# Kernel optimization log

Measured on AMD Instinct MI355X. Metric: run time of the kernel, lower is better.

## Reference

```python
import jax, jax.numpy as jnp
import numpy as np

N = 30000; E = 480000; B = 60
IN = 200; ID = 128; H = 128
NEXP = 4; TOPK = 2; TEMP = 1.5
HEADS = 4; DH = H // HEADS


def _ln(x, g, b):
    mu = jnp.mean(x, -1, keepdims=True)
    var = jnp.var(x, -1, keepdims=True)
    return (x - mu) / jnp.sqrt(var + 1e-5) * g + b


def _seg_sum(d, i, n):
    return jax.ops.segment_sum(d, i, num_segments=n)


def setup_inputs():
    key = jax.random.key(0)
    kit = iter(jax.random.split(key, 80))
    def w(*s):
        return jax.random.normal(next(kit), s, jnp.float32) * 0.05
    inp = {}
    inp['x'] = jax.random.normal(next(kit), (N, IN), jnp.float32)
    inp['node_identity'] = jax.random.normal(next(kit), (N, ID), jnp.float32)
    inp['edge_index'] = jax.random.randint(next(kit), (2, E), 0, N)
    inp['batch'] = jnp.sort(jax.random.randint(next(kit), (N,), 0, B))
    inp.update(fe_W=w(IN, H), fe_b=jnp.zeros(H), fe_g=jnp.ones(H), fe_be=jnp.zeros(H))
    inp.update(ie_W=w(ID, H), ie_b=jnp.zeros(H), ie_g=jnp.ones(H), ie_be=jnp.zeros(H))
    inp.update(fuse_W=w(2 * H, H), fuse_b=jnp.zeros(H), fuse_g=jnp.ones(H), fuse_be=jnp.zeros(H))
    inp.update(router_W=w(2 * H, NEXP))
    inp.update(mlp_W1=w(H, H), mlp_b1=jnp.zeros(H), mlp_W2=w(H, H), mlp_b2=jnp.zeros(H))
    inp.update(cheb_W=w(2, 2, H, H), cheb_b=jnp.zeros((2, H)))
    inp.update(gt_Wq=w(2, H, H), gt_bq=jnp.zeros((2, H)), gt_Wk=w(2, H, H), gt_bk=jnp.zeros((2, H)),
               gt_Wv=w(2, H, H), gt_bv=jnp.zeros((2, H)), gt_Ws=w(2, H, H), gt_bs=jnp.zeros((2, H)))
    inp.update(gcn_W=w(2, H, H), gcn_b=jnp.zeros((2, H)))
    inp.update(pn_g=jnp.ones((NEXP, H)), pn_b=jnp.zeros((NEXP, H)), expert_scales=jnp.ones(NEXP))
    inp.update(h1_W=w(H, H), h1_b=jnp.zeros(H), h1_g=jnp.ones(H), h1_be=jnp.zeros(H))
    inp.update(h2_W=w(H, H // 2), h2_b=jnp.zeros(H // 2), h2_g=jnp.ones(H // 2), h2_be=jnp.zeros(H // 2))
    inp.update(h3_W=w(H // 2, 2), h3_b=jnp.zeros(2), logit_bias=jnp.zeros(2))
    return inp


def _forward(x, node_identity, edge_index, batch, fe_W, fe_b, fe_g, fe_be, ie_W, ie_b, ie_g, ie_be,
             fuse_W, fuse_b, fuse_g, fuse_be, router_W, mlp_W1, mlp_b1, mlp_W2, mlp_b2, cheb_W, cheb_b,
             gt_Wq, gt_bq, gt_Wk, gt_bk, gt_Wv, gt_bv, gt_Ws, gt_bs, gcn_W, gcn_b, pn_g, pn_b,
             expert_scales, h1_W, h1_b, h1_g, h1_be, h2_W, h2_b, h2_g, h2_be, h3_W, h3_b, logit_bias):
    relu = jax.nn.relu
    src, dst = edge_index[0], edge_index[1]
    # encoders + fuse
    h_x = relu(_ln(x @ fe_W + fe_b, fe_g, fe_be))
    h_id = relu(_ln(node_identity @ ie_W + ie_b, ie_g, ie_be))
    h_router = jnp.concatenate([h_x, h_id], -1)
    h = relu(_ln(h_router @ fuse_W + fuse_b, fuse_g, fuse_be))
    # noisy top-k router (eval: no noise, no dropout)
    node_logits = h_router @ router_W
    probs = jax.nn.softmax(node_logits / TEMP, -1)
    vals, idx = jax.lax.top_k(probs, TOPK)
    wts = vals / jnp.clip(jnp.sum(vals, -1, keepdims=True), 1e-9)
    gates = jnp.zeros_like(probs).at[jnp.arange(N)[:, None], idx].set(wts)  # [N, 4]
    # degree / normalization terms
    ones_e = jnp.ones(E, jnp.float32)
    deg = _seg_sum(ones_e, dst, N)
    dinv = jnp.where(deg > 0, jax.lax.rsqrt(jnp.maximum(deg, 1.0)), 0.0)
    dinvl = jax.lax.rsqrt(deg + 1.0)  # with self loops (GCN)
    enorm = dinv[src] * dinv[dst]
    enorml = dinvl[src] * dinvl[dst]
    def aprop(xx, en, di_self=None):
        out = _seg_sum(xx[src] * en[:, None], dst, N)
        if di_self is not None:
            out = out + xx * di_self[:, None]
        return out
    # Expert 0: MLP (2 layers)
    e0 = relu(h @ mlp_W1 + mlp_b1) @ mlp_W2 + mlp_b2
    # Expert 1: ChebNet K=2 (lambda_max=2 -> L_hat = -A_norm), 2 layers
    z = h
    for l in range(2):
        tx1 = -aprop(z, enorm)
        z = z @ cheb_W[l, 0] + tx1 @ cheb_W[l, 1] + cheb_b[l]
        if l == 0:
            z = relu(z)
    e1 = z
    # Expert 2: Graph Transformer, 2 layers, heads=4, root-weight skip
    z = h
    for l in range(2):
        q = (z @ gt_Wq[l] + gt_bq[l]).reshape(N, HEADS, DH)
        k = (z @ gt_Wk[l] + gt_bk[l]).reshape(N, HEADS, DH)
        v = (z @ gt_Wv[l] + gt_bv[l]).reshape(N, HEADS, DH)
        logits = jnp.sum(q[dst] * k[src], -1) * (1.0 / DH ** 0.5)  # [E, heads]
        m = jax.ops.segment_max(logits, dst, num_segments=N)
        m = jnp.where(jnp.isfinite(m), m, 0.0)
        p = jnp.exp(logits - m[dst])
        denom = jnp.clip(_seg_sum(p, dst, N), 1e-9)
        attn = p / denom[dst]
        agg = _seg_sum(attn[:, :, None] * v[src], dst, N).reshape(N, H)
        z = agg + z @ gt_Ws[l] + gt_bs[l]
        if l == 0:
            z = relu(z)
    e2 = z
    # Expert 3: GCN, 2 layers, self loops
    z = h
    for l in range(2):
        zw = z @ gcn_W[l]
        z = aprop(zw, enorml, dinvl * dinvl) + gcn_b[l]
        if l == 0:
            z = relu(z)
    e3 = z
    # per-expert post-norm, scale, gated combine + residual
    eo = jnp.stack([e0, e1, e2, e3], 0)  # [4, N, H]
    eo = _ln(eo, pn_g[:, None, :], pn_b[:, None, :]) * expert_scales[:, None, None]
    out = h + jnp.einsum('ne,enh->nh', gates, eo)
    # mean-pool readout per graph
    counts = jnp.clip(_seg_sum(jnp.ones(N, jnp.float32), batch, B), 1.0)
    pooled = _seg_sum(out, batch, B) / counts[:, None]
    # classification head
    zc = relu(_ln(pooled @ h1_W + h1_b, h1_g, h1_be))
    zc = relu(_ln(zc @ h2_W + h2_b, h2_g, h2_be))
    return zc @ h3_W + h3_b + logit_bias


def reference(x, node_identity, edge_index, batch, fe_W, fe_b, fe_g, fe_be, ie_W, ie_b, ie_g, ie_be,
              fuse_W, fuse_b, fuse_g, fuse_be, router_W, mlp_W1, mlp_b1, mlp_W2, mlp_b2, cheb_W, cheb_b,
              gt_Wq, gt_bq, gt_Wk, gt_bk, gt_Wv, gt_bv, gt_Ws, gt_bs, gcn_W, gcn_b, pn_g, pn_b,
              expert_scales, h1_W, h1_b, h1_g, h1_be, h2_W, h2_b, h2_g, h2_be, h3_W, h3_b, logit_bias):
    return _forward(x, node_identity, edge_index, batch, fe_W, fe_b, fe_g, fe_be, ie_W, ie_b, ie_g, ie_be,
                    fuse_W, fuse_b, fuse_g, fuse_be, router_W, mlp_W1, mlp_b1, mlp_W2, mlp_b2, cheb_W, cheb_b,
                    gt_Wq, gt_bq, gt_Wk, gt_bk, gt_Wv, gt_bv, gt_Ws, gt_bs, gcn_W, gcn_b, pn_g, pn_b,
                    expert_scales, h1_W, h1_b, h1_g, h1_be, h2_W, h2_b, h2_g, h2_be, h3_W, h3_b, logit_bias)
```

## Files before the change

### kernel.cpp

```cpp
#include <hip/hip_runtime.h>

#define RELUF 1
#define ACCF  2
#define LNF   4
#define PCH   32
#define NWT   19
#define SCH   2048

typedef unsigned short ushort_t;
typedef __attribute__((ext_vector_type(8))) short bf16x8;
typedef __attribute__((ext_vector_type(4))) float f32x4;

__device__ __forceinline__ float bf2f(unsigned int v) {
    return __uint_as_float(v << 16);
}
__device__ __forceinline__ unsigned int f2bu(float f) {
    unsigned int u = __float_as_uint(f);
    return (u + 0x7fffu + ((u >> 16) & 1u)) >> 16;
}
__device__ __forceinline__ void unpack8(uint4 u, float* f) {
    f[0] = bf2f(u.x & 0xffff); f[1] = bf2f(u.x >> 16);
    f[2] = bf2f(u.y & 0xffff); f[3] = bf2f(u.y >> 16);
    f[4] = bf2f(u.z & 0xffff); f[5] = bf2f(u.z >> 16);
    f[6] = bf2f(u.w & 0xffff); f[7] = bf2f(u.w >> 16);
}
__device__ __forceinline__ uint4 pack8(const float* f) {
    uint4 p;
    p.x = f2bu(f[0]) | (f2bu(f[1]) << 16);
    p.y = f2bu(f[2]) | (f2bu(f[3]) << 16);
    p.z = f2bu(f[4]) | (f2bu(f[5]) << 16);
    p.w = f2bu(f[6]) | (f2bu(f[7]) << 16);
    return p;
}
__device__ __forceinline__ void fma8(uint4 u, float c, float* a) {
    a[0] = fmaf(c, bf2f(u.x & 0xffff), a[0]);
    a[1] = fmaf(c, bf2f(u.x >> 16), a[1]);
    a[2] = fmaf(c, bf2f(u.y & 0xffff), a[2]);
    a[3] = fmaf(c, bf2f(u.y >> 16), a[3]);
    a[4] = fmaf(c, bf2f(u.z & 0xffff), a[4]);
    a[5] = fmaf(c, bf2f(u.z >> 16), a[5]);
    a[6] = fmaf(c, bf2f(u.w & 0xffff), a[6]);
    a[7] = fmaf(c, bf2f(u.w >> 16), a[7]);
}
__device__ __forceinline__ float dot8(uint4 u, const float* q) {
    float d = q[0] * bf2f(u.x & 0xffff);
    d = fmaf(q[1], bf2f(u.x >> 16), d);
    d = fmaf(q[2], bf2f(u.y & 0xffff), d);
    d = fmaf(q[3], bf2f(u.y >> 16), d);
    d = fmaf(q[4], bf2f(u.z & 0xffff), d);
    d = fmaf(q[5], bf2f(u.z >> 16), d);
    d = fmaf(q[6], bf2f(u.w & 0xffff), d);
    d = fmaf(q[7], bf2f(u.w >> 16), d);
    return d;
}

__global__ void zero2_kernel(int* __restrict__ a, int na, int* __restrict__ b, int nb) {
    int i = blockIdx.x * blockDim.x + threadIdx.x;
    if (i < na) a[i] = 0;
    if (i < nb) b[i] = 0;
}
__global__ void seg_bounds_kernel(const int* __restrict__ batch, int* __restrict__ bstart,
                                  int* __restrict__ bend, int N) {
    int n = blockIdx.x * blockDim.x + threadIdx.x;
    if (n >= N) return;
    int b = batch[n];
    if (n == 0) bstart[b] = 0;
    else {
        int pb = batch[n - 1];
        if (pb != b) { bstart[b] = n; bend[pb] = n; }
    }
    if (n == N - 1) bend[b] = N;
}

__global__ void scan1_kernel(const int* __restrict__ degi, int* __restrict__ rowptr,
                             int* __restrict__ bsum, int n) {
    __shared__ int sh[256];
    int tid = threadIdx.x;
    int base = blockIdx.x * SCH + tid * 8;
    int loc[8]; int s = 0;
#pragma unroll
    for (int j = 0; j < 8; j++) {
        int idx = base + j;
        int v = (idx < n) ? degi[idx] : 0;
        s += v; loc[j] = s;
    }
    sh[tid] = s;
    __syncthreads();
    for (int off = 1; off < 256; off <<= 1) {
        int t = (tid >= off) ? sh[tid - off] : 0;
        __syncthreads();
        sh[tid] += t;
        __syncthreads();
    }
    int prev = (tid > 0) ? sh[tid - 1] : 0;
#pragma unroll
    for (int j = 0; j < 8; j++) {
        int idx = base + j;
        if (idx < n) rowptr[idx + 1] = prev + loc[j];
    }
    if (tid == 255) bsum[blockIdx.x] = sh[255];
}
__global__ void scan2_kernel(int* __restrict__ bsum, int nb) {
    __shared__ int sh[256];
    int tid = threadIdx.x;
    sh[tid] = (tid < nb) ? bsum[tid] : 0;
    __syncthreads();
    for (int off = 1; off < 256; off <<= 1) {
        int t = (tid >= off) ? sh[tid - off] : 0;
        __syncthreads();
        sh[tid] += t;
        __syncthreads();
    }
    if (tid < nb) bsum[tid] = (tid > 0) ? sh[tid - 1] : 0;
}
__global__ void scan3_kernel(int* __restrict__ rowptr, const int* __restrict__ bsum,
                             const int* __restrict__ degi,
                             float* __restrict__ dinv, float* __restrict__ dinvl, int n) {
    int i = blockIdx.x * blockDim.x + threadIdx.x;
    if (i == 0) rowptr[0] = 0;
    if (i < n) {
        rowptr[i + 1] += bsum[i / SCH];
        float deg = (float)degi[i];
        dinv[i] = (deg > 0.f) ? rsqrtf(fmaxf(deg, 1.f)) : 0.f;
        dinvl[i] = rsqrtf(deg + 1.f);
    }
}

struct WtPack {
    const float* src[NWT];
    unsigned long long off[NWT];
    int K[NWT];
};
__global__ void wconv_kernel(WtPack p, ushort_t* __restrict__ base) {
    int a = blockIdx.y;
    const float* s = p.src[a];
    ushort_t* d = base + p.off[a];
    int K = p.K[a];
    int total = K * 128;
    for (int i = blockIdx.x * blockDim.x + threadIdx.x; i < total; i += gridDim.x * blockDim.x) {
        int k = i >> 7, n = i & 127;
        d[n * K + k] = (ushort_t)f2bu(s[i]);
    }
}

__global__ __launch_bounds__(256)
void gemm_f32_ln_kernel(const float* __restrict__ A, int lda, int K,
                        const ushort_t* __restrict__ Wt,
                        ushort_t* __restrict__ Cb,
                        int M,
                        const float* __restrict__ bias,
                        const float* __restrict__ g, const float* __restrict__ be,
                        const float* __restrict__ rW,
                        float* __restrict__ logits)
{
    __shared__ ushort_t As[64][40];
    __shared__ ushort_t Bs[128][40];
    const int tid = threadIdx.x;
    const int m0 = blockIdx.x * 64;
    const int lane = tid & 63;
    const int wv = tid >> 6;
    const int q = lane >> 4;
    const int l16 = lane & 15;
    const int sar = tid >> 2;
    const int sak = (tid & 3) << 3;
    const int sbn = tid >> 1;
    const int sbk = (tid & 1) << 4;
    const bool arow_ok = (m0 + sar) < M;
    const float* Arow = A + (size_t)(m0 + sar) * lda;
    const ushort_t* Wrow = Wt + (size_t)sbn * K;

    f32x4 acc[8];
#pragma unroll
    for (int t = 0; t < 8; t++) acc[t] = (f32x4){0.f, 0.f, 0.f, 0.f};

    for (int k0 = 0; k0 < K; k0 += 32) {
        uint4 apk;
        if (arow_ok && k0 + sak + 8 <= K) {
            float4 p0 = *(const float4*)(Arow + k0 + sak);
            float4 p1 = *(const float4*)(Arow + k0 + sak + 4);
            apk.x = f2bu(p0.x) | (f2bu(p0.y) << 16);
            apk.y = f2bu(p0.z) | (f2bu(p0.w) << 16);
            apk.z = f2bu(p1.x) | (f2bu(p1.y) << 16);
            apk.w = f2bu(p1.z) | (f2bu(p1.w) << 16);
        } else {
            unsigned int t4[4] = {0, 0, 0, 0};
            for (int j = 0; j < 8; j++) {
                int k = k0 + sak + j;
                unsigned int bv = (arow_ok && k < K) ? f2bu(Arow[k]) : 0u;
                t4[j >> 1] |= bv << ((j & 1) * 16);
            }
            apk = make_uint4(t4[0], t4[1], t4[2], t4[3]);
        }
        uint4 b0, b1;
        if (k0 + sbk + 16 <= K) {
            b0 = *(const uint4*)(Wrow + k0 + sbk);
            b1 = *(const uint4*)(Wrow + k0 + sbk + 8);
        } else {
            unsigned int t8[8] = {0, 0, 0, 0, 0, 0, 0, 0};
            for (int j = 0; j < 16; j++) {
                int k = k0 + sbk + j;
                unsigned int bv = (k < K) ? (unsigned int)Wrow[k] : 0u;
                t8[j >> 1] |= bv << ((j & 1) * 16);
            }
            b0 = make_uint4(t8[0], t8[1], t8[2], t8[3]);
            b1 = make_uint4(t8[4], t8[5], t8[6], t8[7]);
        }
        __syncthreads();
        *(uint4*)&As[sar][sak] = apk;
        *(uint4*)&Bs[sbn][sbk] = b0;
        *(uint4*)&Bs[sbn][sbk + 8] = b1;
        __syncthreads();
        bf16x8 af = *(const bf16x8*)&As[16 * wv + l16][q * 8];
#pragma unroll
        for (int t = 0; t < 8; t++) {
            bf16x8 bf = *(const bf16x8*)&Bs[t * 16 + l16][q * 8];
            acc[t] = __builtin_amdgcn_mfma_f32_16x16x32_bf16(af, bf, acc[t], 0, 0, 0);
        }
    }
    const int row_base = m0 + 16 * wv + q * 4;
#pragma unroll
    for (int t = 0; t < 8; t++) {
        float bb = bias[t * 16 + l16];
#pragma unroll
        for (int r = 0; r < 4; r++) acc[t][r] += bb;
    }
    float mean[4], inv[4];
#pragma unroll
    for (int r = 0; r < 4; r++) {
        float s = 0.f, sq = 0.f;
#pragma unroll
        for (int t = 0; t < 8; t++) { float v = acc[t][r]; s += v; sq = fmaf(v, v, sq); }
#pragma unroll
        for (int off = 1; off <= 8; off <<= 1) { s += __shfl_xor(s, off); sq += __shfl_xor(sq, off); }
        mean[r] = s * (1.f / 128.f);
        float var = sq * (1.f / 128.f) - mean[r] * mean[r];
        inv[r] = rsqrtf(var + 1e-5f);
    }
    float rl0[4] = {0, 0, 0, 0}, rl1[4] = {0, 0, 0, 0};
    float rl2[4] = {0, 0, 0, 0}, rl3[4] = {0, 0, 0, 0};
#pragma unroll
    for (int t = 0; t < 8; t++) {
        int col = t * 16 + l16;
        float gg = g[col], b2 = be[col];
        float4 rw = *(const float4*)(rW + col * 4);
#pragma unroll
        for (int r = 0; r < 4; r++) {
            float y = fmaxf(fmaf((acc[t][r] - mean[r]) * inv[r], gg, b2), 0.f);
            rl0[r] = fmaf(y, rw.x, rl0[r]);
            rl1[r] = fmaf(y, rw.y, rl1[r]);
            rl2[r] = fmaf(y, rw.z, rl2[r]);
            rl3[r] = fmaf(y, rw.w, rl3[r]);
            float other = __shfl_xor(y, 1);
            int row = row_base + r;
            if (!(l16 & 1) && row < M) {
                unsigned int pk = f2bu(y) | (f2bu(other) << 16);
                *(unsigned int*)(Cb + (size_t)row * 256 + col) = pk;
            }
        }
    }
#pragma unroll
    for (int r = 0; r < 4; r++) {
#pragma unroll
        for (int off = 1; off <= 8; off <<= 1) {
            rl0[r] += __shfl_xor(rl0[r], off);
            rl1[r] += __shfl_xor(rl1[r], off);
            rl2[r] += __shfl_xor(rl2[r], off);
            rl3[r] += __shfl_xor(rl3[r], off);
        }
        int row = row_base + r;
        if (l16 == 0 && row < M)
            *(float4*)(logits + (size_t)row * 4) = make_float4(rl0[r], rl1[r], rl2[r], rl3[r]);
    }
}

template <int K>
__global__ __launch_bounds__(256)
void gemm_bf_kernel(const ushort_t* __restrict__ A,
                    const ushort_t* __restrict__ Wt,
                    ushort_t* __restrict__ Cb,
                    int M, const float* __restrict__ bias, int flags,
                    const float* __restrict__ g, const float* __restrict__ be)
{
    __shared__ ushort_t As[64][40];
    __shared__ ushort_t Bs[128][40];
    const int tid = threadIdx.x;
    const int m0 = blockIdx.x * 64;
    const int lane = tid & 63;
    const int wv = tid >> 6;
    const int q = lane >> 4;
    const int l16 = lane & 15;
    const int sar = tid >> 2;
    const int sak = (tid & 3) << 3;
    const int sbn = tid >> 1;
    const int sbk = (tid & 1) << 4;
    const bool arow_ok = (m0 + sar) < M;
    const ushort_t* Arow = A + (size_t)(m0 + sar) * K;
    const ushort_t* Wrow = Wt + (size_t)sbn * K;

    f32x4 acc[8];
#pragma unroll
    for (int t = 0; t < 8; t++) acc[t] = (f32x4){0.f, 0.f, 0.f, 0.f};

#pragma unroll
    for (int k0 = 0; k0 < K; k0 += 32) {
        uint4 apk = arow_ok ? *(const uint4*)(Arow + k0 + sak) : make_uint4(0, 0, 0, 0);
        uint4 b0 = *(const uint4*)(Wrow + k0 + sbk);
        uint4 b1 = *(const uint4*)(Wrow + k0 + sbk + 8);
        __syncthreads();
        *(uint4*)&As[sar][sak] = apk;
        *(uint4*)&Bs[sbn][sbk] = b0;
        *(uint4*)&Bs[sbn][sbk + 8] = b1;
        __syncthreads();
        bf16x8 af = *(const bf16x8*)&As[16 * wv + l16][q * 8];
#pragma unroll
        for (int t = 0; t < 8; t++) {
            bf16x8 bf = *(const bf16x8*)&Bs[t * 16 + l16][q * 8];
            acc[t] = __builtin_amdgcn_mfma_f32_16x16x32_bf16(af, bf, acc[t], 0, 0, 0);
        }
    }
    const int row_base = m0 + 16 * wv + q * 4;
    if (flags & LNF) {
#pragma unroll
        for (int t = 0; t < 8; t++) {
            float bb = bias[t * 16 + l16];
#pragma unroll
            for (int r = 0; r < 4; r++) acc[t][r] += bb;
        }
        float mean[4], inv[4];
#pragma unroll
        for (int r = 0; r < 4; r++) {
            float s = 0.f, sq = 0.f;
#pragma unroll
            for (int t = 0; t < 8; t++) { float v = acc[t][r]; s += v; sq = fmaf(v, v, sq); }
#pragma unroll
            for (int off = 1; off <= 8; off <<= 1) { s += __shfl_xor(s, off); sq += __shfl_xor(sq, off); }
            mean[r] = s * (1.f / 128.f);
            float var = sq * (1.f / 128.f) - mean[r] * mean[r];
            inv[r] = rsqrtf(var + 1e-5f);
        }
#pragma unroll
        for (int t = 0; t < 8; t++) {
            int col = t * 16 + l16;
            float gg = g[col], b2 = be[col];
#pragma unroll
            for (int r = 0; r < 4; r++) {
                float y = fmaf((acc[t][r] - mean[r]) * inv[r], gg, b2);
                if (flags & RELUF) y = fmaxf(y, 0.f);
                float other = __shfl_xor(y, 1);
                int row = row_base + r;
                if (!(l16 & 1) && row < M) {
                    unsigned int pk = f2bu(y) | (f2bu(other) << 16);
                    *(unsigned int*)(Cb + (size_t)row * 128 + col) = pk;
                }
            }
        }
        return;
    }
#pragma unroll
    for (int t = 0; t < 8; t++) {
        int col = t * 16 + l16;
        float bb = bias ? bias[col] : 0.f;
#pragma unroll
        for (int r = 0; r < 4; r++) {
            int row = row_base + r;
            bool ok = row < M;
            float val = acc[t][r] + bb;
            if ((flags & ACCF) && ok) val += bf2f(Cb[(size_t)row * 128 + col]);
            if (flags & RELUF) val = fmaxf(val, 0.f);
            float other = __shfl_xor(val, 1);
            if (!(lane & 1) && ok) {
                unsigned int pk = f2bu(val) | (f2bu(other) << 16);
                *(unsigned int*)(Cb + (size_t)row * 128 + col) = pk;
            }
        }
    }
}

__global__ __launch_bounds__(256)
void gemm_dual_kernel(const ushort_t* __restrict__ A1, const ushort_t* __restrict__ Wt1,
                      const ushort_t* __restrict__ A2, const ushort_t* __restrict__ Wt2,
                      ushort_t* __restrict__ Cb, int M,
                      const float* __restrict__ bias, int flags)
{
    const int K = 128;
    __shared__ ushort_t As[64][40];
    __shared__ ushort_t Bs[128][40];
    const int tid = threadIdx.x;
    const int m0 = blockIdx.x * 64;
    const int lane = tid & 63;
    const int wv = tid >> 6;
    const int q = lane >> 4;
    const int l16 = lane & 15;
    const int sar = tid >> 2;
    const int sak = (tid & 3) << 3;
    const int sbn = tid >> 1;
    const int sbk = (tid & 1) << 4;
    const bool arow_ok = (m0 + sar) < M;

    f32x4 acc[8];
#pragma unroll
    for (int t = 0; t < 8; t++) acc[t] = (f32x4){0.f, 0.f, 0.f, 0.f};

    for (int ph = 0; ph < 2; ph++) {
        const ushort_t* Arow = (ph ? A2 : A1) + (size_t)(m0 + sar) * K;
        const ushort_t* Wrow = (ph ? Wt2 : Wt1) + (size_t)sbn * K;
        for (int k0 = 0; k0 < K; k0 += 32) {
            uint4 apk = arow_ok ? *(const uint4*)(Arow + k0 + sak) : make_uint4(0, 0, 0, 0);
            uint4 b0 = *(const uint4*)(Wrow + k0 + sbk);
            uint4 b1 = *(const uint4*)(Wrow + k0 + sbk + 8);
            __syncthreads();
            *(uint4*)&As[sar][sak] = apk;
            *(uint4*)&Bs[sbn][sbk] = b0;
            *(uint4*)&Bs[sbn][sbk + 8] = b1;
            __syncthreads();
            bf16x8 af = *(const bf16x8*)&As[16 * wv + l16][q * 8];
#pragma unroll
            for (int t = 0; t < 8; t++) {
                bf16x8 bf = *(const bf16x8*)&Bs[t * 16 + l16][q * 8];
                acc[t] = __builtin_amdgcn_mfma_f32_16x16x32_bf16(af, bf, acc[t], 0, 0, 0);
            }
        }
    }
#pragma unroll
    for (int t = 0; t < 8; t++) {
        int col = t * 16 + l16;
        float bb = bias ? bias[col] : 0.f;
#pragma unroll
        for (int r = 0; r < 4; r++) {
            int row = m0 + 16 * wv + q * 4 + r;
            bool ok = row < M;
            float val = acc[t][r] + bb;
            if (flags & RELUF) val = fmaxf(val, 0.f);
            float other = __shfl_xor(val, 1);
            if (!(lane & 1) && ok) {
                unsigned int pk = f2bu(val) | (f2bu(other) << 16);
                *(unsigned int*)(Cb + (size_t)row * 128 + col) = pk;
            }
        }
    }
}

__global__ __launch_bounds__(256)
void gemm4_kernel(const ushort_t* __restrict__ A,
                  const ushort_t* __restrict__ Wt,
                  ushort_t* __restrict__ qb,
                  ushort_t* __restrict__ kv,
                  ushort_t* __restrict__ sk,
                  int M,
                  const float* __restrict__ b0, const float* __restrict__ b1,
                  const float* __restrict__ b2, const float* __restrict__ b3)
{
    const int K = 128;
    __shared__ ushort_t As[64][40];
    __shared__ ushort_t Bs[512][40];
    const int tid = threadIdx.x;
    const int m0 = blockIdx.x * 64;
    const int lane = tid & 63;
    const int wv = tid >> 6;
    const int q = lane >> 4;
    const int l16 = lane & 15;
    const int sar = tid >> 2;
    const int sak = (tid & 3) << 3;
    const bool arow_ok = (m0 + sar) < M;
    const ushort_t* Arow = A + (size_t)(m0 + sar) * K;

    f32x4 acc[32];
#pragma unroll
    for (int t = 0; t < 32; t++) acc[t] = (f32x4){0.f, 0.f, 0.f, 0.f};

    for (int k0 = 0; k0 < K; k0 += 32) {
        uint4 apk = arow_ok ? *(const uint4*)(Arow + k0 + sak) : make_uint4(0, 0, 0, 0);
        uint4 bv[4][2];
        int rows[4], kofs[4];
#pragma unroll
        for (int j = 0; j < 4; j++) {
            int slot = tid + j * 256;
            rows[j] = slot >> 1;
            kofs[j] = (slot & 1) << 4;
            const ushort_t* Wrow = Wt + (size_t)rows[j] * K + k0 + kofs[j];
            bv[j][0] = *(const uint4*)Wrow;
            bv[j][1] = *(const uint4*)(Wrow + 8);
        }
        __syncthreads();
        *(uint4*)&As[sar][sak] = apk;
#pragma unroll
        for (int j = 0; j < 4; j++) {
            *(uint4*)&Bs[rows[j]][kofs[j]] = bv[j][0];
            *(uint4*)&Bs[rows[j]][kofs[j] + 8] = bv[j][1];
        }
        __syncthreads();
        bf16x8 af = *(const bf16x8*)&As[16 * wv + l16][q * 8];
#pragma unroll
        for (int t = 0; t < 32; t++) {
            bf16x8 bf = *(const bf16x8*)&Bs[t * 16 + l16][q * 8];
            acc[t] = __builtin_amdgcn_mfma_f32_16x16x32_bf16(af, bf, acc[t], 0, 0, 0);
        }
    }
    const float* bs4[4] = {b0, b1, b2, b3};
#pragma unroll
    for (int s = 0; s < 4; s++) {
#pragma unroll
        for (int t8 = 0; t8 < 8; t8++) {
            int t = s * 8 + t8;
            int col = t8 * 16 + l16;
            float bb = bs4[s][col];
#pragma unroll
            for (int r = 0; r < 4; r++) {
                int row = m0 + 16 * wv + q * 4 + r;
                bool ok = row < M;
                float val = acc[t][r] + bb;
                float other = __shfl_xor(val, 1);
                if (!(lane & 1) && ok) {
                    unsigned int pk = f2bu(val) | (f2bu(other) << 16);
                    if (s == 0)
                        *(unsigned int*)(qb + (size_t)row * 128 + col) = pk;
                    else if (s == 3)
                        *(unsigned int*)(sk + (size_t)row * 128 + col) = pk;
                    else
                        *(unsigned int*)(kv + (size_t)row * 256 + (s - 1) * 128 + col) = pk;
                }
            }
        }
    }
}

__global__ void topk_kernel(const float* __restrict__ la, const float* __restrict__ lb,
                            float* __restrict__ gates, int M)
{
    int n = blockIdx.x * blockDim.x + threadIdx.x;
    if (n >= M) return;
    float4 a = *(const float4*)(la + (size_t)n * 4);
    float4 b = *(const float4*)(lb + (size_t)n * 4);
    float l[4] = {(a.x + b.x) * (1.f / 1.5f), (a.y + b.y) * (1.f / 1.5f),
                  (a.z + b.z) * (1.f / 1.5f), (a.w + b.w) * (1.f / 1.5f)};
    float mx = fmaxf(fmaxf(l[0], l[1]), fmaxf(l[2], l[3]));
    float e[4], ssum = 0.f;
#pragma unroll
    for (int i = 0; i < 4; i++) { e[i] = expf(l[i] - mx); ssum += e[i]; }
    float p[4];
#pragma unroll
    for (int i = 0; i < 4; i++) p[i] = e[i] / ssum;
    int i0 = 0;
    for (int i = 1; i < 4; i++) if (p[i] > p[i0]) i0 = i;
    int i1 = -1;
    for (int i = 0; i < 4; i++) {
        if (i == i0) continue;
        if (i1 < 0 || p[i] > p[i1]) i1 = i;
    }
    float wsum = fmaxf(p[i0] + p[i1], 1e-9f);
    float gg[4] = {0.f, 0.f, 0.f, 0.f};
    gg[i0] = p[i0] / wsum;
    gg[i1] = p[i1] / wsum;
    *(float4*)(gates + (size_t)n * 4) = make_float4(gg[0], gg[1], gg[2], gg[3]);
}

__global__ void edge_deg_kernel(const int* __restrict__ dst, int* __restrict__ degi, int E) {
    int e = blockIdx.x * blockDim.x + threadIdx.x;
    if (e < E) atomicAdd(&degi[dst[e]], 1);
}
__global__ void csr_fill_kernel(const int* __restrict__ src, const int* __restrict__ dst,
                                const int* __restrict__ rowptr, int* __restrict__ cursor,
                                int* __restrict__ csr,
                                const float* __restrict__ dinv, const float* __restrict__ dinvl,
                                float* __restrict__ ecA, float* __restrict__ ecB, int E) {
    int e = blockIdx.x * blockDim.x + threadIdx.x;
    if (e >= E) return;
    int d = dst[e];
    int s = src[e];
    int pos = atomicAdd(&cursor[d], 1);
    int o = rowptr[d] + pos;
    csr[o] = s;
    ecA[o] = dinv[d] * dinv[s];
    ecB[o] = dinvl[d] * dinvl[s];
}

__global__ void gather2_kernel(const ushort_t* __restrict__ Xb,
                               ushort_t* __restrict__ OutA, ushort_t* __restrict__ OutB,
                               const int* __restrict__ rowptr, const int* __restrict__ csr,
                               const float* __restrict__ ecA, const float* __restrict__ ecB,
                               const float* __restrict__ dinvl, int M)
{
    int node = blockIdx.x * 4 + (threadIdx.x >> 6);
    int lane = threadIdx.x & 63;
    if (node >= M) return;
    int beg = rowptr[node], end = rowptr[node + 1];
    int slot = lane >> 4, g = lane & 15;
    float aA[8] = {0, 0, 0, 0, 0, 0, 0, 0};
    float aB[8] = {0, 0, 0, 0, 0, 0, 0, 0};
    int s0 = 0, s1 = 0;
    float cA0 = 0.f, cB0 = 0.f, cA1 = 0.f, cB1 = 0.f;
    {
        int r0 = beg + slot, r1 = beg + 4 + slot;
        if (r0 < end) { s0 = csr[r0]; cA0 = ecA[r0]; cB0 = ecB[r0]; }
        if (r1 < end) { s1 = csr[r1]; cA1 = ecA[r1]; cB1 = ecB[r1]; }
    }
    for (int e = beg; e < end; e += 8) {
        int ns0 = 0, ns1 = 0;
        float nA0 = 0.f, nB0 = 0.f, nA1 = 0.f, nB1 = 0.f;
        int nr0 = e + 8 + slot, nr1 = e + 12 + slot;
        if (nr0 < end) { ns0 = csr[nr0]; nA0 = ecA[nr0]; nB0 = ecB[nr0]; }
        if (nr1 < end) { ns1 = csr[nr1]; nA1 = ecA[nr1]; nB1 = ecB[nr1]; }
        uint4 x0 = *(const uint4*)(Xb + (size_t)s0 * 128 + g * 8);
        uint4 x1 = *(const uint4*)(Xb + (size_t)s1 * 128 + g * 8);
        fma8(x0, cA0, aA); fma8(x0, cB0, aB);
        fma8(x1, cA1, aA); fma8(x1, cB1, aB);
        s0 = ns0; s1 = ns1;
        cA0 = nA0; cB0 = nB0; cA1 = nA1; cB1 = nB1;
    }
#pragma unroll
    for (int j = 0; j < 8; j++) {
        aA[j] += __shfl_xor(aA[j], 16); aA[j] += __shfl_xor(aA[j], 32);
        aB[j] += __shfl_xor(aB[j], 16); aB[j] += __shfl_xor(aB[j], 32);
    }
    {
        float c = dinvl[node]; c *= c;
        uint4 xs = *(const uint4*)(Xb + (size_t)node * 128 + g * 8);
        fma8(xs, c, aB);
    }
    if (lane < 16) {
        float oA[8], oB[8];
#pragma unroll
        for (int j = 0; j < 8; j++) { oA[j] = -aA[j]; oB[j] = aB[j]; }
        size_t ofs = (size_t)node * 128 + g * 8;
        *(uint4*)(OutA + ofs) = pack8(oA);
        *(uint4*)(OutB + ofs) = pack8(oB);
    }
}

__global__ void gather_l2_kernel(const ushort_t* __restrict__ XA, const ushort_t* __restrict__ XB,
                                 ushort_t* __restrict__ OutA, ushort_t* __restrict__ OutB,
                                 const int* __restrict__ rowptr, const int* __restrict__ csr,
                                 const float* __restrict__ ecA, const float* __restrict__ ecB,
                                 const float* __restrict__ dinvl, int M)
{
    int node = blockIdx.x * 4 + (threadIdx.x >> 6);
    int lane = threadIdx.x & 63;
    if (node >= M) return;
    int beg = rowptr[node], end = rowptr[node + 1];
    int slot = lane >> 4, g = lane & 15;
    float aA[8] = {0, 0, 0, 0, 0, 0, 0, 0};
    float aB[8] = {0, 0, 0, 0, 0, 0, 0, 0};
    int s0 = 0, s1 = 0;
    float cA0 = 0.f, cB0 = 0.f, cA1 = 0.f, cB1 = 0.f;
    {
        int r0 = beg + slot, r1 = beg + 4 + slot;
        if (r0 < end) { s0 = csr[r0]; cA0 = ecA[r0]; cB0 = ecB[r0]; }
        if (r1 < end) { s1 = csr[r1]; cA1 = ecA[r1]; cB1 = ecB[r1]; }
    }
    for (int e = beg; e < end; e += 8) {
        int ns0 = 0, ns1 = 0;
        float nA0 = 0.f, nB0 = 0.f, nA1 = 0.f, nB1 = 0.f;
        int nr0 = e + 8 + slot, nr1 = e + 12 + slot;
        if (nr0 < end) { ns0 = csr[nr0]; nA0 = ecA[nr0]; nB0 = ecB[nr0]; }
        if (nr1 < end) { ns1 = csr[nr1]; nA1 = ecA[nr1]; nB1 = ecB[nr1]; }
        uint4 a0 = *(const uint4*)(XA + (size_t)s0 * 128 + g * 8);
        uint4 a1 = *(const uint4*)(XA + (size_t)s1 * 128 + g * 8);
        uint4 b0 = *(const uint4*)(XB + (size_t)s0 * 128 + g * 8);
        uint4 b1 = *(const uint4*)(XB + (size_t)s1 * 128 + g * 8);
        fma8(a0, cA0, aA); fma8(a1, cA1, aA);
        fma8(b0, cB0, aB); fma8(b1, cB1, aB);
        s0 = ns0; s1 = ns1;
        cA0 = nA0; cB0 = nB0; cA1 = nA1; cB1 = nB1;
    }
#pragma unroll
    for (int j = 0; j < 8; j++) {
        aA[j] += __shfl_xor(aA[j], 16); aA[j] += __shfl_xor(aA[j], 32);
        aB[j] += __shfl_xor(aB[j], 16); aB[j] += __shfl_xor(aB[j], 32);
    }
    {
        float c = dinvl[node]; c *= c;
        uint4 xs = *(const uint4*)(XB + (size_t)node * 128 + g * 8);
        fma8(xs, c, aB);
    }
    if (lane < 16) {
        float oA[8], oB[8];
#pragma unroll
        for (int j = 0; j < 8; j++) { oA[j] = -aA[j]; oB[j] = aB[j]; }
        size_t ofs = (size_t)node * 128 + g * 8;
        *(uint4*)(OutA + ofs) = pack8(oA);
        *(uint4*)(OutB + ofs) = pack8(oB);
    }
}

__global__ void gt_attn_kernel(const ushort_t* __restrict__ Qb, const ushort_t* __restrict__ KV,
                               const int* __restrict__ rowptr, const int* __restrict__ csr,
                               const ushort_t* __restrict__ sk, int relu,
                               ushort_t* __restrict__ Outb, int M)
{
    const float SCL = 0.17677669529663689f * 1.4426950408889634f;
    int node = blockIdx.x * 4 + (threadIdx.x >> 6);
    int lane = threadIdx.x & 63;
    if (node >= M) return;
    int beg = rowptr[node], end = rowptr[node + 1];
    int slot = lane >> 4, g = lane & 15;
    uint4 qv = *(const uint4*)(Qb + (size_t)node * 128 + g * 8);
    float qf[8];
    unpack8(qv, qf);
#pragma unroll
    for (int j = 0; j < 8; j++) qf[j] *= SCL;
    float ax[8] = {0, 0, 0, 0, 0, 0, 0, 0};
    float den = 0.f;
    for (int e = beg; e < end; e += 8) {
        int r0 = e + slot, r1 = e + 4 + slot;
        bool v0 = r0 < end, v1 = r1 < end;
        int s0 = 0, s1 = 0;
        if (v0) s0 = csr[r0];
        if (v1) s1 = csr[r1];
        const ushort_t* p0 = KV + (size_t)s0 * 256 + g * 8;
        const ushort_t* p1 = KV + (size_t)s1 * 256 + g * 8;
        uint4 k0 = *(const uint4*)p0;
        uint4 k1 = *(const uint4*)p1;
        uint4 u0 = *(const uint4*)(p0 + 128);
        uint4 u1 = *(const uint4*)(p1 + 128);
        float d0 = dot8(k0, qf);
        float d1 = dot8(k1, qf);
        d0 += __shfl_xor(d0, 1); d0 += __shfl_xor(d0, 2);
        d1 += __shfl_xor(d1, 1); d1 += __shfl_xor(d1, 2);
        float w0 = v0 ? exp2f(fminf(d0, 80.f)) : 0.f;
        float w1 = v1 ? exp2f(fminf(d1, 80.f)) : 0.f;
        den += w0 + w1;
        fma8(u0, w0, ax);
        fma8(u1, w1, ax);
    }
#pragma unroll
    for (int j = 0; j < 8; j++) {
        ax[j] += __shfl_xor(ax[j], 16); ax[j] += __shfl_xor(ax[j], 32);
    }
    den += __shfl_xor(den, 16); den += __shfl_xor(den, 32);
    float dd = fmaxf(den, 1e-9f);
    if (lane < 16) {
        uint4 sv = *(const uint4*)(sk + (size_t)node * 128 + g * 8);
        float sf[8];
        unpack8(sv, sf);
        float o[8];
#pragma unroll
        for (int j = 0; j < 8; j++) {
            float v = ax[j] / dd + sf[j];
            o[j] = relu ? fmaxf(v, 0.f) : v;
        }
        *(uint4*)(Outb + (size_t)node * 128 + g * 8) = pack8(o);
    }
}

__global__ void pool_combine_kernel(const ushort_t* __restrict__ hb,
                                    const ushort_t* __restrict__ e0, const ushort_t* __restrict__ e1,
                                    const ushort_t* __restrict__ e2, const ushort_t* __restrict__ e3,
                                    const float* __restrict__ gates,
                                    const float* __restrict__ png, const float* __restrict__ pnb,
                                    const float* __restrict__ esc,
                                    const int* __restrict__ bstart, const int* __restrict__ bend,
                                    float* __restrict__ partial)
{
    int b = blockIdx.x, c = blockIdx.y;
    int lane = threadIdx.x;
    int s0 = bstart[b], e0i = bend[b];
    const ushort_t* eps[4] = {e0, e1, e2, e3};
    float ga[4], gb[4], ba[4], bb[4], es[4];
#pragma unroll
    for (int ee = 0; ee < 4; ee++) {
        ga[ee] = png[ee * 128 + lane * 2];
        gb[ee] = png[ee * 128 + lane * 2 + 1];
        ba[ee] = pnb[ee * 128 + lane * 2];
        bb[ee] = pnb[ee * 128 + lane * 2 + 1];
        es[ee] = esc[ee];
    }
    float sx = 0.f, sy = 0.f;
    for (int n = s0 + c; n < e0i; n += PCH) {
        size_t ofs = (size_t)n * 128 + lane * 2;
        float4 gg = *(const float4*)(gates + (size_t)n * 4);
        float gv[4] = {gg.x, gg.y, gg.z, gg.w};
        unsigned int hu = *(const unsigned int*)(hb + ofs);
        float ox = bf2f(hu & 0xffff), oy = bf2f(hu >> 16);
#pragma unroll
        for (int ee = 0; ee < 4; ee++) {
            unsigned int u = *(const unsigned int*)(eps[ee] + ofs);
            float vx = bf2f(u & 0xffff), vy = bf2f(u >> 16);
            float su = vx + vy, sq = vx * vx + vy * vy;
#pragma unroll
            for (int off = 32; off; off >>= 1) { su += __shfl_xor(su, off); sq += __shfl_xor(sq, off); }
            float mean = su * (1.f / 128.f);
            float var = sq * (1.f / 128.f) - mean * mean;
            float inv = rsqrtf(var + 1e-5f);
            float cc = es[ee] * gv[ee];
            ox = fmaf(cc, (vx - mean) * inv * ga[ee] + ba[ee], ox);
            oy = fmaf(cc, (vy - mean) * inv * gb[ee] + bb[ee], oy);
        }
        sx += ox; sy += oy;
    }
    *(float2*)(partial + ((size_t)b * PCH + c) * 128 + lane * 2) = make_float2(sx, sy);
}

__global__ void head_kernel(const float* __restrict__ partial,
                            const int* __restrict__ bstart, const int* __restrict__ bend,
                            const float* __restrict__ h1W, const float* __restrict__ h1b,
                            const float* __restrict__ h1g, const float* __restrict__ h1be,
                            const float* __restrict__ h2W, const float* __restrict__ h2b,
                            const float* __restrict__ h2g, const float* __restrict__ h2be,
                            const float* __restrict__ h3W, const float* __restrict__ h3b,
                            const float* __restrict__ lbias,
                            float* __restrict__ out, int B)
{
    __shared__ float p[128], z[128];
    int b = blockIdx.x, t = threadIdx.x;
    float sum = 0.f;
#pragma unroll
    for (int c = 0; c < PCH; c++) sum += partial[((size_t)b * PCH + c) * 128 + t];
    float cnt = fmaxf((float)(bend[b] - bstart[b]), 1.f);
    p[t] = sum / cnt;
    __syncthreads();
    float a = h1b[t];
    for (int k = 0; k < 128; k++) a = fmaf(p[k], h1W[k * 128 + t], a);
    z[t] = a;
    __syncthreads();
    float s = 0.f, sq = 0.f;
    for (int k = 0; k < 128; k++) { float x = z[k]; s += x; sq += x * x; }
    float mean = s * (1.f / 128.f), var = sq * (1.f / 128.f) - mean * mean;
    float y = fmaxf((a - mean) * rsqrtf(var + 1e-5f) * h1g[t] + h1be[t], 0.f);
    __syncthreads();
    z[t] = y;
    __syncthreads();
    float a2 = 0.f;
    if (t < 64) {
        a2 = h2b[t];
        for (int k = 0; k < 128; k++) a2 = fmaf(z[k], h2W[k * 64 + t], a2);
    }
    __syncthreads();
    if (t < 64) p[t] = a2;
    __syncthreads();
    if (t < 2) {
        float s2 = 0.f, sq2 = 0.f;
        for (int k = 0; k < 64; k++) { float x = p[k]; s2 += x; sq2 += x * x; }
        float mean2 = s2 * (1.f / 64.f), var2 = sq2 * (1.f / 64.f) - mean2 * mean2;
        float inv2 = rsqrtf(var2 + 1e-5f);
        float o = h3b[t] + lbias[t];
        for (int k = 0; k < 64; k++) {
            float zc = fmaxf((p[k] - mean2) * inv2 * h2g[k] + h2be[k], 0.f);
            o = fmaf(zc, h3W[k * 2 + t], o);
        }
        out[b * 2 + t] = o;
    }
}

extern "C" void kernel_launch(void* const* d_in, const int* in_sizes, int n_in,
                              void* d_out, int out_size, void* d_ws, size_t ws_size,
                              hipStream_t stream)
{
    (void)ws_size; (void)n_in;
    const int N = in_sizes[3];
    const int E = in_sizes[2] / 2;
    const int B = out_size / 2;

    const int* ei = (const int*)d_in[2];
    const int* src = ei;
    const int* dst = ei + E;
    const int* batch = (const int*)d_in[3];

    const float* W[47];
    for (int i = 0; i < 47; i++) W[i] = (const float*)d_in[i];

    size_t fN = (size_t)N;
    float* gates   = (float*)d_ws;
    float* dinv    = gates + 4 * fN;
    float* dinvl   = dinv + fN;
    float* partial = dinvl + fN;
    float* logitsA = partial + (size_t)128 * B * PCH;
    float* logitsB = logitsA + 4 * fN;
    ushort_t* hb  = (ushort_t*)(logitsB + 4 * fN);
    ushort_t* e0b = hb + 128 * fN;
    ushort_t* e1b = e0b + 128 * fN;
    ushort_t* e2b = e1b + 128 * fN;
    ushort_t* e3b = e2b + 128 * fN;
    ushort_t* x0  = e3b + 128 * fN;
    ushort_t* x1  = x0 + 128 * fN;
    ushort_t* x2  = x1 + 128 * fN;
    ushort_t* x3  = x2 + 128 * fN;
    ushort_t* qb  = x3 + 128 * fN;
    ushort_t* kvb = qb + 128 * fN;
    ushort_t* hrb = kvb + 256 * fN;
    ushort_t* wt  = hrb + 256 * fN;
    WtPack wp;
    const float* wsrc[NWT] = {
        W[4], W[8], W[12], W[17], W[19],
        W[21], W[21] + 16384, W[21] + 32768, W[21] + 49152,
        W[23], W[25], W[27], W[29],
        W[23] + 16384, W[25] + 16384, W[27] + 16384, W[29] + 16384,
        W[31], W[31] + 16384
    };
    const int wk[NWT] = {200, 128, 256, 128, 128,
                         128, 128, 128, 128,
                         128, 128, 128, 128,
                         128, 128, 128, 128,
                         128, 128};
    unsigned long long woff[NWT];
    unsigned long long acc_off = 0;
    for (int i = 0; i < NWT; i++) {
        wp.src[i] = wsrc[i];
        wp.K[i] = wk[i];
        wp.off[i] = acc_off;
        woff[i] = acc_off;
        acc_off += (unsigned long long)128 * wk[i];
    }
    int* degi   = (int*)(wt + acc_off + 8);
    int* cursor = degi + N;
    int* rowptr = cursor + N;
    int* csr    = rowptr + (N + 1);
    int* bstart = csr + E;
    int* bend   = bstart + B;
    int* bsum   = bend + B;
    float* ecA  = (float*)(bsum + 256);
    float* ecB  = ecA + E;

    dim3 blk(256);
    int gN4 = (N + 3) / 4;
    dim3 gG((N + 63) / 64);
    int nsb = (N + SCH - 1) / SCH;

    wconv_kernel<<<dim3(32, NWT), blk, 0, stream>>>(wp, wt);
    zero2_kernel<<<(2 * N + 255) / 256, blk, 0, stream>>>(degi, 2 * N, bstart, 2 * B);
    seg_bounds_kernel<<<(N + 255) / 256, blk, 0, stream>>>(batch, bstart, bend, N);
    edge_deg_kernel<<<(E + 255) / 256, blk, 0, stream>>>(dst, degi, E);
    scan1_kernel<<<dim3(nsb), blk, 0, stream>>>(degi, rowptr, bsum, N);
    scan2_kernel<<<1, blk, 0, stream>>>(bsum, nsb);
    scan3_kernel<<<(N + 255) / 256, blk, 0, stream>>>(rowptr, bsum, degi, dinv, dinvl, N);
    csr_fill_kernel<<<(E + 255) / 256, blk, 0, stream>>>(src, dst, rowptr, cursor, csr,
                                                         dinv, dinvl, ecA, ecB, E);

    gemm_f32_ln_kernel<<<gG, blk, 0, stream>>>(W[0], 200, 200, wt + woff[0], hrb, N,
                                               W[5], W[6], W[7], W[16], logitsA);
    gemm_f32_ln_kernel<<<gG, blk, 0, stream>>>(W[1], 128, 128, wt + woff[1], hrb + 128, N,
                                               W[9], W[10], W[11], W[16] + 512, logitsB);
    topk_kernel<<<(N + 255) / 256, blk, 0, stream>>>(logitsA, logitsB, gates, N);
    gemm_bf_kernel<256><<<gG, blk, 0, stream>>>(hrb, wt + woff[2], hb, N,
                                                W[13], RELUF | LNF, W[14], W[15]);

    gemm_bf_kernel<128><<<gG, blk, 0, stream>>>(hb, wt + woff[3], x0, N, W[18], RELUF, 0, 0);
    gemm_bf_kernel<128><<<gG, blk, 0, stream>>>(x0, wt + woff[4], e0b, N, W[20], 0, 0, 0);

    gather2_kernel<<<gN4, blk, 0, stream>>>(hb, x1, x2, rowptr, csr, ecA, ecB, dinvl, N);

    gemm_dual_kernel<<<gG, blk, 0, stream>>>(hb, wt + woff[5], x1, wt + woff[6],
                                             x0, N, W[22], RELUF);
    gemm_bf_kernel<128><<<gG, blk, 0, stream>>>(x2, wt + woff[17], x1, N, W[32], RELUF, 0, 0);

    gather_l2_kernel<<<gN4, blk, 0, stream>>>(x0, x1, x3, x2, rowptr, csr, ecA, ecB, dinvl, N);

    gemm_dual_kernel<<<gG, blk, 0, stream>>>(x0, wt + woff[7], x3, wt + woff[8],
                                             e1b, N, W[22] + 128, 0);
    gemm_bf_kernel<128><<<gG, blk, 0, stream>>>(x2, wt + woff[18], e3b, N, W[32] + 128, 0, 0, 0);

    gemm4_kernel<<<gG, blk, 0, stream>>>(hb, wt + woff[9], qb, kvb, x3, N,
                                         W[24], W[26], W[28], W[30]);
    gt_attn_kernel<<<gN4, blk, 0, stream>>>(qb, kvb, rowptr, csr, x3, 1, x1, N);
    gemm4_kernel<<<gG, blk, 0, stream>>>(x1, wt + woff[13], qb, kvb, x3, N,
                                         W[24] + 128, W[26] + 128, W[28] + 128, W[30] + 128);
    gt_attn_kernel<<<gN4, blk, 0, stream>>>(qb, kvb, rowptr, csr, x3, 0, e2b, N);

    pool_combine_kernel<<<dim3(B, PCH), dim3(64), 0, stream>>>(
        hb, e0b, e1b, e2b, e3b, gates, W[33], W[34], W[35], bstart, bend, partial);
    head_kernel<<<dim3(B), dim3(128), 0, stream>>>(partial, bstart, bend,
        W[36], W[37], W[38], W[39],
        W[40], W[41], W[42], W[43],
        W[44], W[45], W[46],
        (float*)d_out, B);
}
```

Measured before the change: 580.5 us.

## Merge independent stages into horizontally fused mega-kernels to cut launches

Many small independent kernels (weight conversion, segment bounds, degree count, scan3 plus both encoder GEMMs, CSR fill plus top-k gating, the various expert GEMMs and gathers) are merged into a few kernels that pick their role from the block index. The launch sequence is reordered so that independent branches (GT layer-1 attention with the Chebyshev/GCN layer-2 gather, and the MLP/Cheb/GCN/GT GEMMs) share one launch. Zeroing moves to hipMemsetAsync. This is meant to cut launch overhead and idle tails between dependent launches, at the cost of larger shared memory in the mega GEMM kernels (a 512-row Bs tile), extra intermediate buffers, and possibly lower occupancy for the lighter branches.

```diff
diff --git a/kernel.cpp b/kernel.cpp
--- a/kernel.cpp
+++ b/kernel.cpp
@@ -1,8 +1,5 @@
 #include <hip/hip_runtime.h>
 
-#define RELUF 1
-#define ACCF  2
-#define LNF   4
 #define PCH   32
 #define NWT   19
 #define SCH   2048
@@ -54,22 +51,43 @@
     return d;
 }
 
-__global__ void zero2_kernel(int* __restrict__ a, int na, int* __restrict__ b, int nb) {
-    int i = blockIdx.x * blockDim.x + threadIdx.x;
-    if (i < na) a[i] = 0;
-    if (i < nb) b[i] = 0;
-}
-__global__ void seg_bounds_kernel(const int* __restrict__ batch, int* __restrict__ bstart,
-                                  int* __restrict__ bend, int N) {
-    int n = blockIdx.x * blockDim.x + threadIdx.x;
-    if (n >= N) return;
-    int b = batch[n];
-    if (n == 0) bstart[b] = 0;
-    else {
-        int pb = batch[n - 1];
-        if (pb != b) { bstart[b] = n; bend[pb] = n; }
-    }
-    if (n == N - 1) bend[b] = N;
+struct WtPack {
+    const float* src[NWT];
+    unsigned long long off[NWT];
+    int K[NWT];
+};
+
+__global__ void setup_mega_kernel(WtPack p, ushort_t* __restrict__ base,
+                                  const int* __restrict__ batch,
+                                  int* __restrict__ bstart, int* __restrict__ bend, int N,
+                                  const int* __restrict__ dst, int* __restrict__ degi, int E)
+{
+    int bx = blockIdx.x, tid = threadIdx.x;
+    int nseg = (N + 255) >> 8;
+    if (bx < 608) {
+        int a = bx >> 5, xp = bx & 31;
+        const float* s = p.src[a];
+        ushort_t* d = base + p.off[a];
+        int K = p.K[a];
+        int total = K * 128;
+        for (int i = xp * 256 + tid; i < total; i += 32 * 256) {
+            int k = i >> 7, n = i & 127;
+            d[n * K + k] = (ushort_t)f2bu(s[i]);
+        }
+    } else if (bx < 608 + nseg) {
+        int n = (bx - 608) * 256 + tid;
+        if (n >= N) return;
+        int b = batch[n];
+        if (n == 0) bstart[b] = 0;
+        else {
+            int pb = batch[n - 1];
+            if (pb != b) { bstart[b] = n; bend[pb] = n; }
+        }
+        if (n == N - 1) bend[b] = N;
+    } else {
+        int e = (bx - 608 - nseg) * 256 + tid;
+        if (e < E) atomicAdd(&degi[dst[e]], 1);
+    }
 }
 
 __global__ void scan1_kernel(const int* __restrict__ degi, int* __restrict__ rowptr,
@@ -113,50 +131,19 @@
     }
     if (tid < nb) bsum[tid] = (tid > 0) ? sh[tid - 1] : 0;
 }
-__global__ void scan3_kernel(int* __restrict__ rowptr, const int* __restrict__ bsum,
-                             const int* __restrict__ degi,
-                             float* __restrict__ dinv, float* __restrict__ dinvl, int n) {
-    int i = blockIdx.x * blockDim.x + threadIdx.x;
-    if (i == 0) rowptr[0] = 0;
-    if (i < n) {
-        rowptr[i + 1] += bsum[i / SCH];
-        float deg = (float)degi[i];
-        dinv[i] = (deg > 0.f) ? rsqrtf(fmaxf(deg, 1.f)) : 0.f;
-        dinvl[i] = rsqrtf(deg + 1.f);
-    }
-}
-
-struct WtPack {
-    const float* src[NWT];
-    unsigned long long off[NWT];
-    int K[NWT];
+
+struct EncCfg {
+    const float* A; int lda; int K;
+    const ushort_t* Wt; ushort_t* Cb;
+    const float* bias; const float* g; const float* be;
+    const float* rW; float* logits;
 };
-__global__ void wconv_kernel(WtPack p, ushort_t* __restrict__ base) {
-    int a = blockIdx.y;
-    const float* s = p.src[a];
-    ushort_t* d = base + p.off[a];
-    int K = p.K[a];
-    int total = K * 128;
-    for (int i = blockIdx.x * blockDim.x + threadIdx.x; i < total; i += gridDim.x * blockDim.x) {
-        int k = i >> 7, n = i & 127;
-        d[n * K + k] = (ushort_t)f2bu(s[i]);
-    }
-}
-
-__global__ __launch_bounds__(256)
-void gemm_f32_ln_kernel(const float* __restrict__ A, int lda, int K,
-                        const ushort_t* __restrict__ Wt,
-                        ushort_t* __restrict__ Cb,
-                        int M,
-                        const float* __restrict__ bias,
-                        const float* __restrict__ g, const float* __restrict__ be,
-                        const float* __restrict__ rW,
-                        float* __restrict__ logits)
-{
-    __shared__ ushort_t As[64][40];
-    __shared__ ushort_t Bs[128][40];
+
+__device__ __forceinline__ void gemm_f32_ln_dev(ushort_t (*As)[40], ushort_t (*Bs)[40],
+                                                const EncCfg c, int bx, int M)
+{
     const int tid = threadIdx.x;
-    const int m0 = blockIdx.x * 64;
+    const int m0 = bx * 64;
     const int lane = tid & 63;
     const int wv = tid >> 6;
     const int q = lane >> 4;
@@ -165,9 +152,10 @@
     const int sak = (tid & 3) << 3;
     const int sbn = tid >> 1;
     const int sbk = (tid & 1) << 4;
+    const int K = c.K;
     const bool arow_ok = (m0 + sar) < M;
-    const float* Arow = A + (size_t)(m0 + sar) * lda;
-    const ushort_t* Wrow = Wt + (size_t)sbn * K;
+    const float* Arow = c.A + (size_t)(m0 + sar) * c.lda;
+    const ushort_t* Wrow = c.Wt + (size_t)sbn * K;
 
     f32x4 acc[8];
 #pragma unroll
@@ -220,7 +208,7 @@
     const int row_base = m0 + 16 * wv + q * 4;
 #pragma unroll
     for (int t = 0; t < 8; t++) {
-        float bb = bias[t * 16 + l16];
+        float bb = c.bias[t * 16 + l16];
 #pragma unroll
         for (int r = 0; r < 4; r++) acc[t][r] += bb;
     }
@@ -241,8 +229,8 @@
 #pragma unroll
     for (int t = 0; t < 8; t++) {
         int col = t * 16 + l16;
-        float gg = g[col], b2 = be[col];
-        float4 rw = *(const float4*)(rW + col * 4);
+        float gg = c.g[col], b2 = c.be[col];
+        float4 rw = *(const float4*)(c.rW + col * 4);
 #pragma unroll
         for (int r = 0; r < 4; r++) {
             float y = fmaxf(fmaf((acc[t][r] - mean[r]) * inv[r], gg, b2), 0.f);
@@ -254,7 +242,7 @@
             int row = row_base + r;
             if (!(l16 & 1) && row < M) {
                 unsigned int pk = f2bu(y) | (f2bu(other) << 16);
-                *(unsigned int*)(Cb + (size_t)row * 256 + col) = pk;
+                *(unsigned int*)(c.Cb + (size_t)row * 256 + col) = pk;
             }
         }
     }
@@ -269,18 +257,94 @@
         }
         int row = row_base + r;
         if (l16 == 0 && row < M)
-            *(float4*)(logits + (size_t)row * 4) = make_float4(rl0[r], rl1[r], rl2[r], rl3[r]);
-    }
-}
-
-template <int K>
+            *(float4*)(c.logits + (size_t)row * 4) = make_float4(rl0[r], rl1[r], rl2[r], rl3[r]);
+    }
+}
+
 __global__ __launch_bounds__(256)
-void gemm_bf_kernel(const ushort_t* __restrict__ A,
-                    const ushort_t* __restrict__ Wt,
-                    ushort_t* __restrict__ Cb,
-                    int M, const float* __restrict__ bias, int flags,
-                    const float* __restrict__ g, const float* __restrict__ be)
-{
+void scan3_enc_kernel(int* __restrict__ rowptr, const int* __restrict__ bsum,
+                      const int* __restrict__ degi,
+                      float* __restrict__ dinv, float* __restrict__ dinvl, int N,
+                      EncCfg c0, EncCfg c1)
+{
+    __shared__ ushort_t As[64][40];
+    __shared__ ushort_t Bs[128][40];
+    int bx = blockIdx.x;
+    int ns3 = (N + 255) >> 8;
+    int gG = (N + 63) >> 6;
+    if (bx < ns3) {
+        int i = bx * 256 + threadIdx.x;
+        if (i == 0) rowptr[0] = 0;
+        if (i < N) {
+            rowptr[i + 1] += bsum[i / SCH];
+            float deg = (float)degi[i];
+            dinv[i] = (deg > 0.f) ? rsqrtf(fmaxf(deg, 1.f)) : 0.f;
+            dinvl[i] = rsqrtf(deg + 1.f);
+        }
+        return;
+    }
+    int b2 = bx - ns3;
+    if (b2 < gG) gemm_f32_ln_dev(As, Bs, c0, b2, N);
+    else gemm_f32_ln_dev(As, Bs, c1, b2 - gG, N);
+}
+
+__global__ void csr_topk_kernel(const int* __restrict__ src, const int* __restrict__ dst,
+                                const int* __restrict__ rowptr, int* __restrict__ cursor,
+                                int* __restrict__ csr,
+                                const float* __restrict__ dinv, const float* __restrict__ dinvl,
+                                float* __restrict__ ecA, float* __restrict__ ecB, int E,
+                                const float* __restrict__ la, const float* __restrict__ lb,
+                                float* __restrict__ gates, int N)
+{
+    int bx = blockIdx.x;
+    int nc = (E + 255) >> 8;
+    if (bx < nc) {
+        int e = bx * 256 + threadIdx.x;
+        if (e >= E) return;
+        int d = dst[e];
+        int s = src[e];
+        int pos = atomicAdd(&cursor[d], 1);
+        int o = rowptr[d] + pos;
+        csr[o] = s;
+        ecA[o] = dinv[d] * dinv[s];
+        ecB[o] = dinvl[d] * dinvl[s];
+        return;
+    }
+    int n = (bx - nc) * 256 + threadIdx.x;
+    if (n >= N) return;
+    float4 a = *(const float4*)(la + (size_t)n * 4);
+    float4 b = *(const float4*)(lb + (size_t)n * 4);
+    float l[4] = {(a.x + b.x) * (1.f / 1.5f), (a.y + b.y) * (1.f / 1.5f),
+                  (a.z + b.z) * (1.f / 1.5f), (a.w + b.w) * (1.f / 1.5f)};
+    float mx = fmaxf(fmaxf(l[0], l[1]), fmaxf(l[2], l[3]));
+    float e4[4], ssum = 0.f;
+#pragma unroll
+    for (int i = 0; i < 4; i++) { e4[i] = expf(l[i] - mx); ssum += e4[i]; }
+    float p[4];
+#pragma unroll
+    for (int i = 0; i < 4; i++) p[i] = e4[i] / ssum;
+    int i0 = 0;
+    for (int i = 1; i < 4; i++) if (p[i] > p[i0]) i0 = i;
+    int i1 = -1;
+    for (int i = 0; i < 4; i++) {
+        if (i == i0) continue;
+        if (i1 < 0 || p[i] > p[i1]) i1 = i;
+    }
+    float wsum = fmaxf(p[i0] + p[i1], 1e-9f);
+    float gg[4] = {0.f, 0.f, 0.f, 0.f};
+    gg[i0] = p[i0] / wsum;
+    gg[i1] = p[i1] / wsum;
+    *(float4*)(gates + (size_t)n * 4) = make_float4(gg[0], gg[1], gg[2], gg[3]);
+}
+
+__global__ __launch_bounds__(256)
+void gemm_ln256_kernel(const ushort_t* __restrict__ A,
+                       const ushort_t* __restrict__ Wt,
+                       ushort_t* __restrict__ Cb, int M,
+                       const float* __restrict__ bias,
+                       const float* __restrict__ g, const float* __restrict__ be)
+{
+    const int K = 256;
     __shared__ ushort_t As[64][40];
     __shared__ ushort_t Bs[128][40];
     const int tid = threadIdx.x;
@@ -319,42 +383,82 @@
         }
     }
     const int row_base = m0 + 16 * wv + q * 4;
-    if (flags & LNF) {
+#pragma unroll
+    for (int t = 0; t < 8; t++) {
+        float bb = bias[t * 16 + l16];
+#pragma unroll
+        for (int r = 0; r < 4; r++) acc[t][r] += bb;
+    }
+    float mean[4], inv[4];
+#pragma unroll
+    for (int r = 0; r < 4; r++) {
+        float s = 0.f, sq = 0.f;
+#pragma unroll
+        for (int t = 0; t < 8; t++) { float v = acc[t][r]; s += v; sq = fmaf(v, v, sq); }
+#pragma unroll
+        for (int off = 1; off <= 8; off <<= 1) { s += __shfl_xor(s, off); sq += __shfl_xor(sq, off); }
+        mean[r] = s * (1.f / 128.f);
+        float var = sq * (1.f / 128.f) - mean[r] * mean[r];
+        inv[r] = rsqrtf(var + 1e-5f);
+    }
+#pragma unroll
+    for (int t = 0; t < 8; t++) {
+        int col = t * 16 + l16;
+        float gg = g[col], b2 = be[col];
+#pragma unroll
+        for (int r = 0; r < 4; r++) {
+            float y = fmaxf(fmaf((acc[t][r] - mean[r]) * inv[r], gg, b2), 0.f);
+            float other = __shfl_xor(y, 1);
+            int row = row_base + r;
+            if (!(l16 & 1) && row < M) {
+                unsigned int pk = f2bu(y) | (f2bu(other) << 16);
+                *(unsigned int*)(Cb + (size_t)row * 128 + col) = pk;
+            }
+        }
+    }
+}
+
+template <int K>
+__device__ __forceinline__ void gemm_bf_dev(ushort_t (*As)[40], ushort_t (*Bs)[40],
+                                            const ushort_t* __restrict__ A,
+                                            const ushort_t* __restrict__ Wt,
+                                            ushort_t* __restrict__ Cb, int M,
+                                            const float* __restrict__ bias, int relu, int bx)
+{
+    const int tid = threadIdx.x;
+    const int m0 = bx * 64;
+    const int lane = tid & 63;
+    const int wv = tid >> 6;
+    const int q = lane >> 4;
+    const int l16 = lane & 15;
+    const int sar = tid >> 2;
+    const int sak = (tid & 3) << 3;
+    const int sbn = tid >> 1;
+    const int sbk = (tid & 1) << 4;
+    const bool arow_ok = (m0 + sar) < M;
+    const ushort_t* Arow = A + (size_t)(m0 + sar) * K;
+    const ushort_t* Wrow = Wt + (size_t)sbn * K;
+
+    f32x4 acc[8];
+#pragma unroll
+    for (int t = 0; t < 8; t++) acc[t] = (f32x4){0.f, 0.f, 0.f, 0.f};
+
+#pragma unroll
+    for (int k0 = 0; k0 < K; k0 += 32) {
+        uint4 apk = arow_ok ? *(const uint4*)(Arow + k0 + sak) : make_uint4(0, 0, 0, 0);
+        uint4 b0 = *(const uint4*)(Wrow + k0 + sbk);
+        uint4 b1 = *(const uint4*)(Wrow + k0 + sbk + 8);
+        __syncthreads();
+        *(uint4*)&As[sar][sak] = apk;
+        *(uint4*)&Bs[sbn][sbk] = b0;
+        *(uint4*)&Bs[sbn][sbk + 8] = b1;
+        __syncthreads();
+        bf16x8 af = *(const bf16x8*)&As[16 * wv + l16][q * 8];
 #pragma unroll
         for (int t = 0; t < 8; t++) {
-            float bb = bias[t * 16 + l16];
-#pragma unroll
-            for (int r = 0; r < 4; r++) acc[t][r] += bb;
-        }
-        float mean[4], inv[4];
-#pragma unroll
-        for (int r = 0; r < 4; r++) {
-            float s = 0.f, sq = 0.f;
-#pragma unroll
-            for (int t = 0; t < 8; t++) { float v = acc[t][r]; s += v; sq = fmaf(v, v, sq); }
-#pragma unroll
-            for (int off = 1; off <= 8; off <<= 1) { s += __shfl_xor(s, off); sq += __shfl_xor(sq, off); }
-            mean[r] = s * (1.f / 128.f);
-            float var = sq * (1.f / 128.f) - mean[r] * mean[r];
-            inv[r] = rsqrtf(var + 1e-5f);
-        }
-#pragma unroll
-        for (int t = 0; t < 8; t++) {
-            int col = t * 16 + l16;
-            float gg = g[col], b2 = be[col];
-#pragma unroll
-            for (int r = 0; r < 4; r++) {
-                float y = fmaf((acc[t][r] - mean[r]) * inv[r], gg, b2);
-                if (flags & RELUF) y = fmaxf(y, 0.f);
-                float other = __shfl_xor(y, 1);
-                int row = row_base + r;
-                if (!(l16 & 1) && row < M) {
-                    unsigned int pk = f2bu(y) | (f2bu(other) << 16);
-                    *(unsigned int*)(Cb + (size_t)row * 128 + col) = pk;
-                }
-            }
-        }
-        return;
+            bf16x8 bf = *(const bf16x8*)&Bs[t * 16 + l16][q * 8];
+            acc[t] = __builtin_amdgcn_mfma_f32_16x16x32_bf16(af, bf, acc[t], 0, 0, 0);
+        }
     }
 #pragma unroll
     for (int t = 0; t < 8; t++) {
@@ -362,13 +466,11 @@
         float bb = bias ? bias[col] : 0.f;
 #pragma unroll
         for (int r = 0; r < 4; r++) {
-            int row = row_base + r;
-            bool ok = row < M;
+            int row = m0 + 16 * wv + q * 4 + r;
             float val = acc[t][r] + bb;
-            if ((flags & ACCF) && ok) val += bf2f(Cb[(size_t)row * 128 + col]);
-            if (flags & RELUF) val = fmaxf(val, 0.f);
+            if (relu) val = fmaxf(val, 0.f);
             float other = __shfl_xor(val, 1);
-            if (!(lane & 1) && ok) {
+            if (!(lane & 1) && row < M) {
                 unsigned int pk = f2bu(val) | (f2bu(other) << 16);
                 *(unsigned int*)(Cb + (size_t)row * 128 + col) = pk;
             }
@@ -376,17 +478,17 @@
     }
 }
 
-__global__ __launch_bounds__(256)
-void gemm_dual_kernel(const ushort_t* __restrict__ A1, const ushort_t* __restrict__ Wt1,
-                      const ushort_t* __restrict__ A2, const ushort_t* __restrict__ Wt2,
-                      ushort_t* __restrict__ Cb, int M,
-                      const float* __restrict__ bias, int flags)
+__device__ __forceinline__ void gemm_dual_dev(ushort_t (*As)[40], ushort_t (*Bs)[40],
+                                              const ushort_t* __restrict__ A1,
+                                              const ushort_t* __restrict__ Wt1,
+                                              const ushort_t* __restrict__ A2,
+                                              const ushort_t* __restrict__ Wt2,
+                                              ushort_t* __restrict__ Cb, int M,
+                                              const float* __restrict__ bias, int relu, int bx)
 {
     const int K = 128;
-    __shared__ ushort_t As[64][40];
-    __shared__ ushort_t Bs[128][40];
     const int tid = threadIdx.x;
-    const int m0 = blockIdx.x * 64;
+    const int m0 = bx * 64;
     const int lane = tid & 63;
     const int wv = tid >> 6;
     const int q = lane >> 4;
@@ -428,11 +530,10 @@
 #pragma unroll
         for (int r = 0; r < 4; r++) {
             int row = m0 + 16 * wv + q * 4 + r;
-            bool ok = row < M;
             float val = acc[t][r] + bb;
-            if (flags & RELUF) val = fmaxf(val, 0.f);
+            if (relu) val = fmaxf(val, 0.f);
             float other = __shfl_xor(val, 1);
-            if (!(lane & 1) && ok) {
+            if (!(lane & 1) && row < M) {
                 unsigned int pk = f2bu(val) | (f2bu(other) << 16);
                 *(unsigned int*)(Cb + (size_t)row * 128 + col) = pk;
             }
@@ -440,21 +541,18 @@
     }
 }
 
-__global__ __launch_bounds__(256)
-void gemm4_kernel(const ushort_t* __restrict__ A,
-                  const ushort_t* __restrict__ Wt,
-                  ushort_t* __restrict__ qb,
-                  ushort_t* __restrict__ kv,
-                  ushort_t* __restrict__ sk,
-                  int M,
-                  const float* __restrict__ b0, const float* __restrict__ b1,
-                  const float* __restrict__ b2, const float* __restrict__ b3)
+__device__ __forceinline__ void gemm4_dev(ushort_t (*As)[40], ushort_t (*Bs)[40],
+                                          const ushort_t* __restrict__ A,
+                                          const ushort_t* __restrict__ Wt,
+                                          ushort_t* __restrict__ qb, ushort_t* __restrict__ kv,
+                                          ushort_t* __restrict__ sk, int M,
+                                          const float* __restrict__ b0, const float* __restrict__ b1,
+                                          const float* __restrict__ b2, const float* __restrict__ b3,
+                                          int bx)
 {
     const int K = 128;
-    __shared__ ushort_t As[64][40];
-    __shared__ ushort_t Bs[512][40];
     const int tid = threadIdx.x;
-    const int m0 = blockIdx.x * 64;
+    const int m0 = bx * 64;
     const int lane = tid & 63;
     const int wv = tid >> 6;
     const int q = lane >> 4;
@@ -507,10 +605,9 @@
 #pragma unroll
             for (int r = 0; r < 4; r++) {
                 int row = m0 + 16 * wv + q * 4 + r;
-                bool ok = row < M;
                 float val = acc[t][r] + bb;
                 float other = __shfl_xor(val, 1);
-                if (!(lane & 1) && ok) {
+                if (!(lane & 1) && row < M) {
                     unsigned int pk = f2bu(val) | (f2bu(other) << 16);
                     if (s == 0)
                         *(unsigned int*)(qb + (size_t)row * 128 + col) = pk;
@@ -524,63 +621,59 @@
     }
 }
 
-__global__ void topk_kernel(const float* __restrict__ la, const float* __restrict__ lb,
-                            float* __restrict__ gates, int M)
-{
-    int n = blockIdx.x * blockDim.x + threadIdx.x;
-    if (n >= M) return;
-    float4 a = *(const float4*)(la + (size_t)n * 4);
-    float4 b = *(const float4*)(lb + (size_t)n * 4);
-    float l[4] = {(a.x + b.x) * (1.f / 1.5f), (a.y + b.y) * (1.f / 1.5f),
-                  (a.z + b.z) * (1.f / 1.5f), (a.w + b.w) * (1.f / 1.5f)};
-    float mx = fmaxf(fmaxf(l[0], l[1]), fmaxf(l[2], l[3]));
-    float e[4], ssum = 0.f;
-#pragma unroll
-    for (int i = 0; i < 4; i++) { e[i] = expf(l[i] - mx); ssum += e[i]; }
-    float p[4];
-#pragma unroll
-    for (int i = 0; i < 4; i++) p[i] = e[i] / ssum;
-    int i0 = 0;
-    for (int i = 1; i < 4; i++) if (p[i] > p[i0]) i0 = i;
-    int i1 = -1;
-    for (int i = 0; i < 4; i++) {
-        if (i == i0) continue;
-        if (i1 < 0 || p[i] > p[i1]) i1 = i;
-    }
-    float wsum = fmaxf(p[i0] + p[i1], 1e-9f);
-    float gg[4] = {0.f, 0.f, 0.f, 0.f};
-    gg[i0] = p[i0] / wsum;
-    gg[i1] = p[i1] / wsum;
-    *(float4*)(gates + (size_t)n * 4) = make_float4(gg[0], gg[1], gg[2], gg[3]);
-}
-
-__global__ void edge_deg_kernel(const int* __restrict__ dst, int* __restrict__ degi, int E) {
-    int e = blockIdx.x * blockDim.x + threadIdx.x;
-    if (e < E) atomicAdd(&degi[dst[e]], 1);
-}
-__global__ void csr_fill_kernel(const int* __restrict__ src, const int* __restrict__ dst,
-                                const int* __restrict__ rowptr, int* __restrict__ cursor,
-                                int* __restrict__ csr,
-                                const float* __restrict__ dinv, const float* __restrict__ dinvl,
-                                float* __restrict__ ecA, float* __restrict__ ecB, int E) {
-    int e = blockIdx.x * blockDim.x + threadIdx.x;
-    if (e >= E) return;
-    int d = dst[e];
-    int s = src[e];
-    int pos = atomicAdd(&cursor[d], 1);
-    int o = rowptr[d] + pos;
-    csr[o] = s;
-    ecA[o] = dinv[d] * dinv[s];
-    ecB[o] = dinvl[d] * dinvl[s];
-}
-
-__global__ void gather2_kernel(const ushort_t* __restrict__ Xb,
-                               ushort_t* __restrict__ OutA, ushort_t* __restrict__ OutB,
-                               const int* __restrict__ rowptr, const int* __restrict__ csr,
-                               const float* __restrict__ ecA, const float* __restrict__ ecB,
-                               const float* __restrict__ dinvl, int M)
-{
-    int node = blockIdx.x * 4 + (threadIdx.x >> 6);
+__device__ __forceinline__ void gemm_wv_dev(const ushort_t* __restrict__ A,
+                                            const ushort_t* __restrict__ Wt,
+                                            ushort_t* __restrict__ Cb, int M,
+                                            const float* __restrict__ bias, int relu,
+                                            int w, int lane)
+{
+    const int K = 128;
+    int ct = w & 3;
+    int rt = w >> 2;
+    int row0 = rt * 16;
+    if (row0 >= M) return;
+    int l16 = lane & 15, q = lane >> 4;
+    int arow = row0 + l16;
+    bool aok = arow < M;
+    const ushort_t* Ar = A + (size_t)arow * K + q * 8;
+    const ushort_t* W0 = Wt + (size_t)(ct * 32 + l16) * K + q * 8;
+    const ushort_t* W1 = W0 + (size_t)16 * K;
+    bf16x8 zz = {0, 0, 0, 0, 0, 0, 0, 0};
+    f32x4 a0 = {0.f, 0.f, 0.f, 0.f}, a1 = {0.f, 0.f, 0.f, 0.f};
+#pragma unroll
+    for (int k0 = 0; k0 < K; k0 += 32) {
+        bf16x8 af = aok ? *(const bf16x8*)(Ar + k0) : zz;
+        bf16x8 b0 = *(const bf16x8*)(W0 + k0);
+        bf16x8 b1 = *(const bf16x8*)(W1 + k0);
+        a0 = __builtin_amdgcn_mfma_f32_16x16x32_bf16(af, b0, a0, 0, 0, 0);
+        a1 = __builtin_amdgcn_mfma_f32_16x16x32_bf16(af, b1, a1, 0, 0, 0);
+    }
+    f32x4 av[2] = {a0, a1};
+#pragma unroll
+    for (int t = 0; t < 2; t++) {
+        int col = ct * 32 + t * 16 + l16;
+        float bb = bias ? bias[col] : 0.f;
+#pragma unroll
+        for (int r = 0; r < 4; r++) {
+            int row = row0 + q * 4 + r;
+            float val = av[t][r] + bb;
+            if (relu) val = fmaxf(val, 0.f);
+            float other = __shfl_xor(val, 1);
+            if (!(l16 & 1) && row < M) {
+                unsigned int pk = f2bu(val) | (f2bu(other) << 16);
+                *(unsigned int*)(Cb + (size_t)row * 128 + col) = pk;
+            }
+        }
+    }
+}
+
+__device__ __forceinline__ void gather2_dev(const ushort_t* __restrict__ Xb,
+                                            ushort_t* __restrict__ OutA, ushort_t* __restrict__ OutB,
+                                            const int* __restrict__ rowptr, const int* __restrict__ csr,
+                                            const float* __restrict__ ecA, const float* __restrict__ ecB,
+                                            const float* __restrict__ dinvl, int M, int bx)
+{
+    int node = bx * 4 + (threadIdx.x >> 6);
     int lane = threadIdx.x & 63;
     if (node >= M) return;
     int beg = rowptr[node], end = rowptr[node + 1];
@@ -627,13 +720,14 @@
     }
 }
 
-__global__ void gather_l2_kernel(const ushort_t* __restrict__ XA, const ushort_t* __restrict__ XB,
-                                 ushort_t* __restrict__ OutA, ushort_t* __restrict__ OutB,
-                                 const int* __restrict__ rowptr, const int* __restrict__ csr,
-                                 const float* __restrict__ ecA, const float* __restrict__ ecB,
-                                 const float* __restrict__ dinvl, int M)
-{
-    int node = blockIdx.x * 4 + (threadIdx.x >> 6);
+__device__ __forceinline__ void gather_l2_dev(const ushort_t* __restrict__ XA,
+                                              const ushort_t* __restrict__ XB,
+                                              ushort_t* __restrict__ OutA, ushort_t* __restrict__ OutB,
+                                              const int* __restrict__ rowptr, const int* __restrict__ csr,
+                                              const float* __restrict__ ecA, const float* __restrict__ ecB,
+                                              const float* __restrict__ dinvl, int M, int bx)
+{
+    int node = bx * 4 + (threadIdx.x >> 6);
     int lane = threadIdx.x & 63;
     if (node >= M) return;
     int beg = rowptr[node], end = rowptr[node + 1];
@@ -682,13 +776,14 @@
     }
 }
 
-__global__ void gt_attn_kernel(const ushort_t* __restrict__ Qb, const ushort_t* __restrict__ KV,
-                               const int* __restrict__ rowptr, const int* __restrict__ csr,
-                               const ushort_t* __restrict__ sk, int relu,
-                               ushort_t* __restrict__ Outb, int M)
+__device__ __forceinline__ void gt_attn_dev(const ushort_t* __restrict__ Qb,
+                                            const ushort_t* __restrict__ KV,
+                                            const int* __restrict__ rowptr, const int* __restrict__ csr,
+                                            const ushort_t* __restrict__ sk, int relu,
+                                            ushort_t* __restrict__ Outb, int M, int bx)
 {
     const float SCL = 0.17677669529663689f * 1.4426950408889634f;
-    int node = blockIdx.x * 4 + (threadIdx.x >> 6);
+    int node = bx * 4 + (threadIdx.x >> 6);
     int lane = threadIdx.x & 63;
     if (node >= M) return;
     int beg = rowptr[node], end = rowptr[node + 1];
@@ -742,6 +837,91 @@
     }
 }
 
+__global__ void flatA_kernel(const ushort_t* __restrict__ hb,
+                             ushort_t* __restrict__ x1, ushort_t* __restrict__ x2,
+                             const int* __restrict__ rowptr, const int* __restrict__ csr,
+                             const float* __restrict__ ecA, const float* __restrict__ ecB,
+                             const float* __restrict__ dinvl, int N,
+                             const ushort_t* __restrict__ wmlp1, ushort_t* __restrict__ xm,
+                             const float* __restrict__ b18)
+{
+    int bx = blockIdx.x;
+    int gN4 = (N + 3) >> 2;
+    if (bx < gN4) {
+        gather2_dev(hb, x1, x2, rowptr, csr, ecA, ecB, dinvl, N, bx);
+    } else {
+        int w = (bx - gN4) * 4 + (threadIdx.x >> 6);
+        gemm_wv_dev(hb, wmlp1, xm, N, b18, 1, w, threadIdx.x & 63);
+    }
+}
+
+__global__ __launch_bounds__(256)
+void megaA_kernel(const ushort_t* __restrict__ hb,
+                  const ushort_t* __restrict__ wqkvs,
+                  ushort_t* __restrict__ qb, ushort_t* __restrict__ kvb, ushort_t* __restrict__ skb,
+                  const float* __restrict__ bq, const float* __restrict__ bk,
+                  const float* __restrict__ bv, const float* __restrict__ bs,
+                  const ushort_t* __restrict__ x1, const ushort_t* __restrict__ wch0,
+                  const ushort_t* __restrict__ wch1, ushort_t* __restrict__ x0,
+                  const float* __restrict__ bch,
+                  const ushort_t* __restrict__ x2, const ushort_t* __restrict__ wgcn,
+                  ushort_t* __restrict__ xg1, const float* __restrict__ bgcn,
+                  int M)
+{
+    __shared__ ushort_t As[64][40];
+    __shared__ ushort_t Bs[512][40];
+    int y = blockIdx.y, bx = blockIdx.x;
+    if (y == 0) gemm4_dev(As, Bs, hb, wqkvs, qb, kvb, skb, M, bq, bk, bv, bs, bx);
+    else if (y == 1) gemm_dual_dev(As, Bs, hb, wch0, x1, wch1, x0, M, bch, 1, bx);
+    else gemm_bf_dev<128>(As, Bs, x2, wgcn, xg1, M, bgcn, 1, bx);
+}
+
+__global__ void flatB_kernel(const ushort_t* __restrict__ qb, const ushort_t* __restrict__ kvb,
+                             const int* __restrict__ rowptr, const int* __restrict__ csr,
+                             const ushort_t* __restrict__ skb, ushort_t* __restrict__ aout,
+                             const ushort_t* __restrict__ x0, const ushort_t* __restrict__ xg1,
+                             ushort_t* __restrict__ x3, ushort_t* __restrict__ x2,
+                             const float* __restrict__ ecA, const float* __restrict__ ecB,
+                             const float* __restrict__ dinvl, int N)
+{
+    int bx = blockIdx.x;
+    int gN4 = (N + 3) >> 2;
+    if (bx < gN4) gt_attn_dev(qb, kvb, rowptr, csr, skb, 1, aout, N, bx);
+    else gather_l2_dev(x0, xg1, x3, x2, rowptr, csr, ecA, ecB, dinvl, N, bx - gN4);
+}
+
+__global__ __launch_bounds__(256)
+void megaB_kernel(const ushort_t* __restrict__ x1,
+                  const ushort_t* __restrict__ wqkvs,
+                  ushort_t* __restrict__ qb, ushort_t* __restrict__ kvb, ushort_t* __restrict__ skb,
+                  const float* __restrict__ bq, const float* __restrict__ bk,
+                  const float* __restrict__ bv, const float* __restrict__ bs,
+                  const ushort_t* __restrict__ x0, const ushort_t* __restrict__ wch0,
+                  const ushort_t* __restrict__ x3, const ushort_t* __restrict__ wch1,
+                  ushort_t* __restrict__ e1b, const float* __restrict__ bch,
+                  const ushort_t* __restrict__ x2, const ushort_t* __restrict__ wgcn,
+                  ushort_t* __restrict__ e3b, const float* __restrict__ bgcn,
+                  const ushort_t* __restrict__ xm, const ushort_t* __restrict__ wmlp2,
+                  ushort_t* __restrict__ e0b, const float* __restrict__ bmlp2,
+                  int M)
+{
+    __shared__ ushort_t As[64][40];
+    __shared__ ushort_t Bs[512][40];
+    int y = blockIdx.y, bx = blockIdx.x;
+    if (y == 0) gemm4_dev(As, Bs, x1, wqkvs, qb, kvb, skb, M, bq, bk, bv, bs, bx);
+    else if (y == 1) gemm_dual_dev(As, Bs, x0, wch0, x3, wch1, e1b, M, bch, 0, bx);
+    else if (y == 2) gemm_bf_dev<128>(As, Bs, x2, wgcn, e3b, M, bgcn, 0, bx);
+    else gemm_bf_dev<128>(As, Bs, xm, wmlp2, e0b, M, bmlp2, 0, bx);
+}
+
+__global__ void gt_attn2_kernel(const ushort_t* __restrict__ Qb, const ushort_t* __restrict__ KV,
+                                const int* __restrict__ rowptr, const int* __restrict__ csr,
+                                const ushort_t* __restrict__ sk,
+                                ushort_t* __restrict__ Outb, int M)
+{
+    gt_attn_dev(Qb, KV, rowptr, csr, sk, 0, Outb, M, blockIdx.x);
+}
+
 __global__ void pool_combine_kernel(const ushort_t* __restrict__ hb,
                                     const ushort_t* __restrict__ e0, const ushort_t* __restrict__ e1,
                                     const ushort_t* __restrict__ e2, const ushort_t* __restrict__ e3,
@@ -874,7 +1054,10 @@
     ushort_t* x1  = x0 + 128 * fN;
     ushort_t* x2  = x1 + 128 * fN;
     ushort_t* x3  = x2 + 128 * fN;
-    ushort_t* qb  = x3 + 128 * fN;
+    ushort_t* xm  = x3 + 128 * fN;
+    ushort_t* xg1 = xm + 128 * fN;
+    ushort_t* skb = xg1 + 128 * fN;
+    ushort_t* qb  = skb + 128 * fN;
     ushort_t* kvb = qb + 128 * fN;
     ushort_t* hrb = kvb + 256 * fN;
     ushort_t* wt  = hrb + 256 * fN;
@@ -912,49 +1095,44 @@
 
     dim3 blk(256);
     int gN4 = (N + 3) / 4;
-    dim3 gG((N + 63) / 64);
+    int gG = (N + 63) / 64;
+    int RT = (N + 15) / 16;
     int nsb = (N + SCH - 1) / SCH;
-
-    wconv_kernel<<<dim3(32, NWT), blk, 0, stream>>>(wp, wt);
-    zero2_kernel<<<(2 * N + 255) / 256, blk, 0, stream>>>(degi, 2 * N, bstart, 2 * B);
-    seg_bounds_kernel<<<(N + 255) / 256, blk, 0, stream>>>(batch, bstart, bend, N);
-    edge_deg_kernel<<<(E + 255) / 256, blk, 0, stream>>>(dst, degi, E);
+    int nseg = (N + 255) / 256;
+    int nedge = (E + 255) / 256;
+
+    hipMemsetAsync(degi, 0, (size_t)2 * N * sizeof(int), stream);
+    hipMemsetAsync(bstart, 0, (size_t)2 * B * sizeof(int), stream);
+
+    setup_mega_kernel<<<dim3(608 + nseg + nedge), blk, 0, stream>>>(
+        wp, wt, batch, bstart, bend, N, dst, degi, E);
     scan1_kernel<<<dim3(nsb), blk, 0, stream>>>(degi, rowptr, bsum, N);
     scan2_kernel<<<1, blk, 0, stream>>>(bsum, nsb);
-    scan3_kernel<<<(N + 255) / 256, blk, 0, stream>>>(rowptr, bsum, degi, dinv, dinvl, N);
-    csr_fill_kernel<<<(E + 255) / 256, blk, 0, stream>>>(src, dst, rowptr, cursor, csr,
-                                                         dinv, dinvl, ecA, ecB, E);
-
-    gemm_f32_ln_kernel<<<gG, blk, 0, stream>>>(W[0], 200, 200, wt + woff[0], hrb, N,
-                                               W[5], W[6], W[7], W[16], logitsA);
-    gemm_f32_ln_kernel<<<gG, blk, 0, stream>>>(W[1], 128, 128, wt + woff[1], hrb + 128, N,
-                                               W[9], W[10], W[11], W[16] + 512, logitsB);
-    topk_kernel<<<(N + 255) / 256, blk, 0, stream>>>(logitsA, logitsB, gates, N);
-    gemm_bf_kernel<256><<<gG, blk, 0, stream>>>(hrb, wt + woff[2], hb, N,
-                                                W[13], RELUF | LNF, W[14], W[15]);
-
-    gemm_bf_kernel<128><<<gG, blk, 0, stream>>>(hb, wt + woff[3], x0, N, W[18], RELUF, 0, 0);
-    gemm_bf_kernel<128><<<gG, blk, 0, stream>>>(x0, wt + woff[4], e0b, N, W[20], 0, 0, 0);
-
-    gather2_kernel<<<gN4, blk, 0, stream>>>(hb, x1, x2, rowptr, csr, ecA, ecB, dinvl, N);
-
-    gemm_dual_kernel<<<gG, blk, 0, stream>>>(hb, wt + woff[5], x1, wt + woff[6],
-                                             x0, N, W[22], RELUF);
-    gemm_bf_kernel<128><<<gG, blk, 0, stream>>>(x2, wt + woff[17], x1, N, W[32], RELUF, 0, 0);
-
-    gather_l2_kernel<<<gN4, blk, 0, stream>>>(x0, x1, x3, x2, rowptr, csr, ecA, ecB, dinvl, N);
-
-    gemm_dual_kernel<<<gG, blk, 0, stream>>>(x0, wt + woff[7], x3, wt + woff[8],
-                                             e1b, N, W[22] + 128, 0);
-    gemm_bf_kernel<128><<<gG, blk, 0, stream>>>(x2, wt + woff[18], e3b, N, W[32] + 128, 0, 0, 0);
-
-    gemm4_kernel<<<gG, blk, 0, stream>>>(hb, wt + woff[9], qb, kvb, x3, N,
-                                         W[24], W[26], W[28], W[30]);
-    gt_attn_kernel<<<gN4, blk, 0, stream>>>(qb, kvb, rowptr, csr, x3, 1, x1, N);
-    gemm4_kernel<<<gG, blk, 0, stream>>>(x1, wt + woff[13], qb, kvb, x3, N,
-                                         W[24] + 128, W[26] + 128, W[28] + 128, W[30] + 128);
-    gt_attn_kernel<<<gN4, blk, 0, stream>>>(qb, kvb, rowptr, csr, x3, 0, e2b, N);
-
+    EncCfg c0 = {W[0], 200, 200, wt + woff[0], hrb, W[5], W[6], W[7], W[16], logitsA};
+    EncCfg c1 = {W[1], 128, 128, wt + woff[1], hrb + 128, W[9], W[10], W[11], W[16] + 512, logitsB};
+    scan3_enc_kernel<<<dim3(nseg + 2 * gG), blk, 0, stream>>>(
+        rowptr, bsum, degi, dinv, dinvl, N, c0, c1);
+    csr_topk_kernel<<<dim3(nedge + nseg), blk, 0, stream>>>(
+        src, dst, rowptr, cursor, csr, dinv, dinvl, ecA, ecB, E,
+        logitsA, logitsB, gates, N);
+    gemm_ln256_kernel<<<dim3(gG), blk, 0, stream>>>(hrb, wt + woff[2], hb, N,
+                                                    W[13], W[14], W[15]);
+    flatA_kernel<<<dim3(gN4 + RT), blk, 0, stream>>>(hb, x1, x2, rowptr, csr, ecA, ecB,
+                                                     dinvl, N, wt + woff[3], xm, W[18]);
+    megaA_kernel<<<dim3(gG, 3), blk, 0, stream>>>(
+        hb, wt + woff[9], qb, kvb, skb, W[24], W[26], W[28], W[30],
+        x1, wt + woff[5], wt + woff[6], x0, W[22],
+        x2, wt + woff[17], xg1, W[32], N);
+    flatB_kernel<<<dim3(2 * gN4), blk, 0, stream>>>(
+        qb, kvb, rowptr, csr, skb, x1,
+        x0, xg1, x3, x2, ecA, ecB, dinvl, N);
+    megaB_kernel<<<dim3(gG, 4), blk, 0, stream>>>(
+        x1, wt + woff[13], qb, kvb, skb,
+        W[24] + 128, W[26] + 128, W[28] + 128, W[30] + 128,
+        x0, wt + woff[7], x3, wt + woff[8], e1b, W[22] + 128,
+        x2, wt + woff[18], e3b, W[32] + 128,
+        xm, wt + woff[4], e0b, W[20], N);
+    gt_attn2_kernel<<<dim3(gN4), blk, 0, stream>>>(qb, kvb, rowptr, csr, skb, e2b, N);
     pool_combine_kernel<<<dim3(B, PCH), dim3(64), 0, stream>>>(
         hb, e0b, e1b, e2b, e3b, gates, W[33], W[34], W[35], bstart, bend, partial);
     head_kernel<<<dim3(B), dim3(128), 0, stream>>>(partial, bstart, bend,
```

Result: faster. 554.6 us (-4.5%).
